# Performance work log

Measured on AMD Instinct MI355X. Metric: run time of the kernel, lower is better.

The kernel has to match this reference:

```python
import jax, jax.numpy as jnp
import numpy as np

T, N, H, W = 1, 2048, 512, 512
CHUNK = 128  # gaussians per scan step; intermediate alpha is (CHUNK,H,W) ~ 128MB fp32


def setup_inputs() -> dict:
    key = jax.random.key(0)
    k1, k2, k3, k4 = jax.random.split(key, 4)
    # matches torch init: atanh(2*(rand-0.5)) so tanh(xyz) is uniform in (-1,1)
    u = jax.random.uniform(k1, (T, N, 2), dtype=jnp.float32, minval=1e-4, maxval=1.0 - 1e-4)
    xyz = jnp.arctanh(2.0 * (u - 0.5))
    # cholesky params near identity: [1,0,1] + 0.01*randn
    cholesky = jnp.array([1.0, 0.0, 1.0], jnp.float32).reshape(1, 1, 3) \
        + 0.01 * jax.random.normal(k2, (T, N, 3), dtype=jnp.float32)
    opacity = jnp.ones((N, 1), jnp.float32)
    features_dc = jax.random.normal(k4, (N, 3), dtype=jnp.float32)
    return {"xyz": xyz, "cholesky": cholesky, "opacity": opacity,
            "features_dc": features_dc, "frame_index": 0}


def _render_frame(means, chol, colors, opac):
    """Accumulated-summation 2D Gaussian splat (GaussianImage rasterize_gaussians_sum).

    means: (N,2) in (-1,1); chol: (N,3) Cholesky elems (l11,l21,l22);
    colors: (N,3) in (0,1); opac: (N,) in (0,1). Returns (3,H,W).
    """
    l1, l2, l3 = chol[:, 0], chol[:, 1], chol[:, 2]
    # Sigma = L L^T with L = [[l1,0],[l2,l3]]
    s11 = l1 * l1
    s12 = l1 * l2
    s22 = l2 * l2 + l3 * l3
    det = s11 * s22 - s12 * s12
    conic = jnp.stack([s22 / det, -s12 / det, s11 / det], axis=-1)  # (N,3) inverse cov
    # project to pixel coords
    xys = 0.5 * (means + 1.0) * jnp.array([W, H], means.dtype)  # (N,2)

    px = jnp.arange(W, dtype=means.dtype) + 0.5  # pixel centers
    py = jnp.arange(H, dtype=means.dtype) + 0.5

    steps = N // CHUNK
    xs = (xys.reshape(steps, CHUNK, 2), conic.reshape(steps, CHUNK, 3),
          colors.reshape(steps, CHUNK, 3), opac.reshape(steps, CHUNK))

    def body(img, args):
        xy, cc, col, op = args
        dx = xy[:, 0, None] - px[None, :]          # (C,W)
        dy = xy[:, 1, None] - py[None, :]          # (C,H)
        sigma = (0.5 * cc[:, 0, None, None] * (dx[:, None, :] ** 2)
                 + 0.5 * cc[:, 2, None, None] * (dy[:, :, None] ** 2)
                 + cc[:, 1, None, None] * dy[:, :, None] * dx[:, None, :])  # (C,H,W)
        alpha = op[:, None, None] * jnp.exp(-sigma)
        alpha = jnp.where(sigma < 0.0, 0.0, jnp.minimum(alpha, 0.999))
        alpha = jnp.where(alpha < 1.0 / 255.0, 0.0, alpha)  # kernel skip threshold
        img = img + jnp.einsum('chw,ck->khw', alpha, col)
        return img, None

    img0 = jnp.zeros((3, H, W), means.dtype)
    img, _ = jax.lax.scan(body, img0, xs)
    return img


def reference(xyz, cholesky, opacity, features_dc, frame_index):
    cholesky_bound = jnp.array([0.5, 0.0, 0.5], xyz.dtype)
    means_t = jnp.tanh(xyz[frame_index])                       # (N,2)
    chol_t = cholesky[frame_index] + cholesky_bound            # (N,3)
    colors = jax.nn.sigmoid(features_dc)                       # (N,3)
    opac = jax.nn.sigmoid(opacity[:, 0])                       # (N,)
    img = _render_frame(means_t, chol_t, colors, opac)
    img = jnp.clip(img, 0.0, 1.0)
    return img[None]  # (1,3,H,W)
```

## Files before the change

### kernel.cpp

```cpp
#include <hip/hip_runtime.h>
#include <math.h>

#define N_GAUSS 2048
#define IMG_H 512
#define IMG_W 512

__global__ void zero_kernel(float4* __restrict__ out, int n4) {
    int i = blockIdx.x * blockDim.x + threadIdx.x;
    if (i < n4) out[i] = make_float4(0.f, 0.f, 0.f, 0.f);
}

__global__ __launch_bounds__(64) void splat_kernel(
    const float* __restrict__ xyz,
    const float* __restrict__ chol,
    const float* __restrict__ opacity,
    const float* __restrict__ fdc,
    float* __restrict__ out)
{
    const int g = blockIdx.x;
    const int lane = threadIdx.x;

    float mx = tanhf(xyz[2 * g]);
    float my = tanhf(xyz[2 * g + 1]);
    float l1 = chol[3 * g]     + 0.5f;
    float l2 = chol[3 * g + 1];
    float l3 = chol[3 * g + 2] + 0.5f;

    float s11 = l1 * l1;
    float s12 = l1 * l2;
    float s22 = l2 * l2 + l3 * l3;
    float det = s11 * s22 - s12 * s12;
    float inv = 1.0f / det;
    float c0 =  s22 * inv;
    float c1 = -s12 * inv;
    float c2 =  s11 * inv;

    float cx = 0.5f * (mx + 1.0f) * (float)IMG_W;
    float cy = 0.5f * (my + 1.0f) * (float)IMG_H;

    float op = 1.0f / (1.0f + expf(-opacity[g]));
    float cr = 1.0f / (1.0f + expf(-fdc[3 * g]));
    float cg = 1.0f / (1.0f + expf(-fdc[3 * g + 1]));
    float cb = 1.0f / (1.0f + expf(-fdc[3 * g + 2]));

    float s_max = logf(255.0f * op);
    if (s_max < 0.0f) return;

    float rx = sqrtf(2.0f * s_max * s11) + 1.0f;
    float ry = sqrtf(2.0f * s_max * s22) + 1.0f;

    int w0 = max(0,         (int)floorf(cx - rx - 0.5f));
    int w1 = min(IMG_W - 1, (int)ceilf (cx + rx - 0.5f));
    int h0 = max(0,         (int)floorf(cy - ry - 0.5f));
    int h1 = min(IMG_H - 1, (int)ceilf (cy + ry - 0.5f));
    if (w1 < w0 || h1 < h0) return;

    int bw  = w1 - w0 + 1;
    int bh  = h1 - h0 + 1;
    int tot = bw * bh;

    for (int idx = lane; idx < tot; idx += 64) {
        int h = h0 + idx / bw;
        int w = w0 + idx % bw;
        float dx = cx - ((float)w + 0.5f);
        float dy = cy - ((float)h + 0.5f);
        float sigma = 0.5f * c0 * dx * dx + 0.5f * c2 * dy * dy + c1 * dy * dx;
        if (sigma < 0.0f) continue;
        float alpha = fminf(op * expf(-sigma), 0.999f);
        if (alpha < (1.0f / 255.0f)) continue;
        int p = h * IMG_W + w;
        atomicAdd(&out[0 * IMG_H * IMG_W + p], alpha * cr);
        atomicAdd(&out[1 * IMG_H * IMG_W + p], alpha * cg);
        atomicAdd(&out[2 * IMG_H * IMG_W + p], alpha * cb);
    }
}

__global__ void clip_kernel(float4* __restrict__ out, int n4) {
    int i = blockIdx.x * blockDim.x + threadIdx.x;
    if (i < n4) {
        float4 v = out[i];
        v.x = fminf(fmaxf(v.x, 0.0f), 1.0f);
        v.y = fminf(fmaxf(v.y, 0.0f), 1.0f);
        v.z = fminf(fmaxf(v.z, 0.0f), 1.0f);
        v.w = fminf(fmaxf(v.w, 0.0f), 1.0f);
        out[i] = v;
    }
}

extern "C" void kernel_launch(void* const* d_in, const int* in_sizes, int n_in,
                              void* d_out, int out_size, void* d_ws, size_t ws_size,
                              hipStream_t stream) {
    const float* xyz     = (const float*)d_in[0];
    const float* chol    = (const float*)d_in[1];
    const float* opacity = (const float*)d_in[2];
    const float* fdc     = (const float*)d_in[3];

    float* out = (float*)d_out;
    int n4 = out_size / 4;

    zero_kernel<<<(n4 + 255) / 256, 256, 0, stream>>>((float4*)out, n4);
    splat_kernel<<<N_GAUSS, 64, 0, stream>>>(xyz, chol, opacity, fdc, out);
    clip_kernel<<<(n4 + 255) / 256, 256, 0, stream>>>((float4*)out, n4);
}
```

Before: 71.79 us.

## Replace atomic per-Gaussian splatting with per-tile Gaussian binning and register accumulation

Switches from one block per Gaussian scattering atomicAdds into global memory to one block per 64x4 pixel tile. Each tile first culls all Gaussians against its bounding box into a shared-memory list with cached parameters, then every pixel accumulates color in registers and writes the clipped result once. This drops the zero and clip kernels and all global atomics. In exchange every tile redundantly evaluates all 2048 Gaussians for culling, and Gaussians beyond the 512-entry cache are recomputed from global memory. Summation order is now sequential per pixel rather than atomic order.

```diff
diff --git a/kernel.cpp b/kernel.cpp
--- a/kernel.cpp
+++ b/kernel.cpp
@@ -4,87 +4,127 @@
 #define N_GAUSS 2048
 #define IMG_H 512
 #define IMG_W 512
+#define TILE_W 64
+#define TILE_H 4
+#define TILES_X (IMG_W / TILE_W)
+#define TILES_Y (IMG_H / TILE_H)
+#define N_TILES (TILES_X * TILES_Y)
+#define PCACHE 512
 
-__global__ void zero_kernel(float4* __restrict__ out, int n4) {
-    int i = blockIdx.x * blockDim.x + threadIdx.x;
-    if (i < n4) out[i] = make_float4(0.f, 0.f, 0.f, 0.f);
-}
-
-__global__ __launch_bounds__(64) void splat_kernel(
+__global__ __launch_bounds__(256) void splat_tiled(
     const float* __restrict__ xyz,
     const float* __restrict__ chol,
     const float* __restrict__ opacity,
     const float* __restrict__ fdc,
     float* __restrict__ out)
 {
-    const int g = blockIdx.x;
-    const int lane = threadIdx.x;
+    __shared__ int   s_count;
+    __shared__ int   s_idx[N_GAUSS];
+    __shared__ float s_par[PCACHE][9];
 
-    float mx = tanhf(xyz[2 * g]);
-    float my = tanhf(xyz[2 * g + 1]);
-    float l1 = chol[3 * g]     + 0.5f;
-    float l2 = chol[3 * g + 1];
-    float l3 = chol[3 * g + 2] + 0.5f;
+    const int tile = blockIdx.x;
+    const int tx = tile % TILES_X;
+    const int ty = tile / TILES_X;
+    const int t  = threadIdx.x;
 
-    float s11 = l1 * l1;
-    float s12 = l1 * l2;
-    float s22 = l2 * l2 + l3 * l3;
-    float det = s11 * s22 - s12 * s12;
-    float inv = 1.0f / det;
-    float c0 =  s22 * inv;
-    float c1 = -s12 * inv;
-    float c2 =  s11 * inv;
+    const float x0 = (float)(tx * TILE_W) + 0.5f;
+    const float x1 = (float)(tx * TILE_W + TILE_W - 1) + 0.5f;
+    const float y0 = (float)(ty * TILE_H) + 0.5f;
+    const float y1 = (float)(ty * TILE_H + TILE_H - 1) + 0.5f;
 
-    float cx = 0.5f * (mx + 1.0f) * (float)IMG_W;
-    float cy = 0.5f * (my + 1.0f) * (float)IMG_H;
+    if (t == 0) s_count = 0;
+    __syncthreads();
 
-    float op = 1.0f / (1.0f + expf(-opacity[g]));
-    float cr = 1.0f / (1.0f + expf(-fdc[3 * g]));
-    float cg = 1.0f / (1.0f + expf(-fdc[3 * g + 1]));
-    float cb = 1.0f / (1.0f + expf(-fdc[3 * g + 2]));
+    for (int g = t; g < N_GAUSS; g += 256) {
+        float mx = tanhf(xyz[2 * g]);
+        float my = tanhf(xyz[2 * g + 1]);
+        float cx = 0.5f * (mx + 1.0f) * (float)IMG_W;
+        float cy = 0.5f * (my + 1.0f) * (float)IMG_H;
 
-    float s_max = logf(255.0f * op);
-    if (s_max < 0.0f) return;
+        float l1 = chol[3 * g]     + 0.5f;
+        float l2 = chol[3 * g + 1];
+        float l3 = chol[3 * g + 2] + 0.5f;
+        float s11 = l1 * l1;
+        float s22 = l2 * l2 + l3 * l3;
 
-    float rx = sqrtf(2.0f * s_max * s11) + 1.0f;
-    float ry = sqrtf(2.0f * s_max * s22) + 1.0f;
+        float op = 1.0f / (1.0f + __expf(-opacity[g]));
+        float smax = __logf(255.0f * op);
+        if (smax <= 0.0f) continue;
 
-    int w0 = max(0,         (int)floorf(cx - rx - 0.5f));
-    int w1 = min(IMG_W - 1, (int)ceilf (cx + rx - 0.5f));
-    int h0 = max(0,         (int)floorf(cy - ry - 0.5f));
-    int h1 = min(IMG_H - 1, (int)ceilf (cy + ry - 0.5f));
-    if (w1 < w0 || h1 < h0) return;
+        float rx = sqrtf(2.0f * smax * s11) + 1.0f;
+        float ry = sqrtf(2.0f * smax * s22) + 1.0f;
 
-    int bw  = w1 - w0 + 1;
-    int bh  = h1 - h0 + 1;
-    int tot = bw * bh;
+        if (cx + rx < x0 || cx - rx > x1 || cy + ry < y0 || cy - ry > y1)
+            continue;
 
-    for (int idx = lane; idx < tot; idx += 64) {
-        int h = h0 + idx / bw;
-        int w = w0 + idx % bw;
-        float dx = cx - ((float)w + 0.5f);
-        float dy = cy - ((float)h + 0.5f);
+        int pos = atomicAdd(&s_count, 1);
+        s_idx[pos] = g;
+        if (pos < PCACHE) {
+            float s12 = l1 * l2;
+            float det = s11 * s22 - s12 * s12;
+            float inv = 1.0f / det;
+            s_par[pos][0] = cx;
+            s_par[pos][1] = cy;
+            s_par[pos][2] =  s22 * inv;
+            s_par[pos][3] = -s12 * inv;
+            s_par[pos][4] =  s11 * inv;
+            s_par[pos][5] = 1.0f / (1.0f + expf(-opacity[g]));
+            s_par[pos][6] = 1.0f / (1.0f + expf(-fdc[3 * g]));
+            s_par[pos][7] = 1.0f / (1.0f + expf(-fdc[3 * g + 1]));
+            s_par[pos][8] = 1.0f / (1.0f + expf(-fdc[3 * g + 2]));
+        }
+    }
+    __syncthreads();
+
+    const int w = tx * TILE_W + (t & (TILE_W - 1));
+    const int h = ty * TILE_H + (t >> 6);
+    const float px = (float)w + 0.5f;
+    const float py = (float)h + 0.5f;
+
+    float R = 0.0f, G = 0.0f, B = 0.0f;
+    const int cnt = s_count;
+    for (int i = 0; i < cnt; i++) {
+        float cx, cy, c0, c1, c2, op, cr, cg, cb;
+        if (i < PCACHE) {
+            cx = s_par[i][0]; cy = s_par[i][1];
+            c0 = s_par[i][2]; c1 = s_par[i][3]; c2 = s_par[i][4];
+            op = s_par[i][5];
+            cr = s_par[i][6]; cg = s_par[i][7]; cb = s_par[i][8];
+        } else {
+            int g = s_idx[i];
+            float mx = tanhf(xyz[2 * g]);
+            float my = tanhf(xyz[2 * g + 1]);
+            cx = 0.5f * (mx + 1.0f) * (float)IMG_W;
+            cy = 0.5f * (my + 1.0f) * (float)IMG_H;
+            float l1 = chol[3 * g]     + 0.5f;
+            float l2 = chol[3 * g + 1];
+            float l3 = chol[3 * g + 2] + 0.5f;
+            float s11 = l1 * l1;
+            float s12 = l1 * l2;
+            float s22 = l2 * l2 + l3 * l3;
+            float det = s11 * s22 - s12 * s12;
+            float inv = 1.0f / det;
+            c0 =  s22 * inv; c1 = -s12 * inv; c2 = s11 * inv;
+            op = 1.0f / (1.0f + expf(-opacity[g]));
+            cr = 1.0f / (1.0f + expf(-fdc[3 * g]));
+            cg = 1.0f / (1.0f + expf(-fdc[3 * g + 1]));
+            cb = 1.0f / (1.0f + expf(-fdc[3 * g + 2]));
+        }
+        float dx = cx - px;
+        float dy = cy - py;
         float sigma = 0.5f * c0 * dx * dx + 0.5f * c2 * dy * dy + c1 * dy * dx;
         if (sigma < 0.0f) continue;
         float alpha = fminf(op * expf(-sigma), 0.999f);
         if (alpha < (1.0f / 255.0f)) continue;
-        int p = h * IMG_W + w;
-        atomicAdd(&out[0 * IMG_H * IMG_W + p], alpha * cr);
-        atomicAdd(&out[1 * IMG_H * IMG_W + p], alpha * cg);
-        atomicAdd(&out[2 * IMG_H * IMG_W + p], alpha * cb);
+        R += alpha * cr;
+        G += alpha * cg;
+        B += alpha * cb;
     }
-}
 
-__global__ void clip_kernel(float4* __restrict__ out, int n4) {
-    int i = blockIdx.x * blockDim.x + threadIdx.x;
-    if (i < n4) {
-        float4 v = out[i];
-        v.x = fminf(fmaxf(v.x, 0.0f), 1.0f);
-        v.y = fminf(fmaxf(v.y, 0.0f), 1.0f);
-        v.z = fminf(fmaxf(v.z, 0.0f), 1.0f);
-        v.w = fminf(fmaxf(v.w, 0.0f), 1.0f);
-        out[i] = v;
-    }
+    const int p = h * IMG_W + w;
+    out[p]                     = fminf(fmaxf(R, 0.0f), 1.0f);
+    out[IMG_H * IMG_W + p]     = fminf(fmaxf(G, 0.0f), 1.0f);
+    out[2 * IMG_H * IMG_W + p] = fminf(fmaxf(B, 0.0f), 1.0f);
 }
 
 extern "C" void kernel_launch(void* const* d_in, const int* in_sizes, int n_in,
@@ -96,9 +136,6 @@
     const float* fdc     = (const float*)d_in[3];
 
     float* out = (float*)d_out;
-    int n4 = out_size / 4;
 
-    zero_kernel<<<(n4 + 255) / 256, 256, 0, stream>>>((float4*)out, n4);
-    splat_kernel<<<N_GAUSS, 64, 0, stream>>>(xyz, chol, opacity, fdc, out);
-    clip_kernel<<<(n4 + 255) / 256, 256, 0, stream>>>((float4*)out, n4);
+    splat_tiled<<<N_TILES, 256, 0, stream>>>(xyz, chol, opacity, fdc, out);
 }
```

After: 79.64 us. +10.9%, slower.
